# Kernel optimization log

Hardware: AMD Instinct MI355X
Metric: run time of the kernel (lower is better)

The kernel has to match this reference:

```python
import jax, jax.numpy as jnp
import numpy as np

BS, L, D, H, NL, ITEM_NUM = 128, 64, 512, 8, 2, 100000
NEG_INF = -10000.0


def _ln(x):
    m = jnp.mean(x, axis=-1, keepdims=True)
    v = jnp.var(x, axis=-1, keepdims=True)
    return (x - m) * jax.lax.rsqrt(v + 1e-5)


def _user_encoder(input_embs, log_mask, pos_emb, qkv_w, out_w, ffn_w1, ffn_w2):
    # SASRec-style causal transformer encoder (post-LN blocks)
    B, S, d = input_embs.shape
    dh = d // H
    x = _ln(input_embs + pos_emb[None, :, :])
    pad = (log_mask != 0)                                  # [B,S]
    causal = jnp.tril(jnp.ones((S, S), dtype=bool))
    attn_ok = causal[None, :, :] & pad[:, None, :]         # [B,S,S]
    bias = jnp.where(attn_ok, 0.0, NEG_INF)[:, None, :, :]  # [B,1,S,S]
    for l in range(NL):
        qkv = x @ qkv_w[l]                                 # [B,S,3d]
        q, k, v = jnp.split(qkv, 3, axis=-1)
        q = q.reshape(B, S, H, dh).transpose(0, 2, 1, 3)
        k = k.reshape(B, S, H, dh).transpose(0, 2, 1, 3)
        v = v.reshape(B, S, H, dh).transpose(0, 2, 1, 3)
        scores = jnp.einsum('bhqd,bhkd->bhqk', q, k) / jnp.sqrt(jnp.asarray(dh, x.dtype)) + bias
        attn = jax.nn.softmax(scores, axis=-1)
        o = jnp.einsum('bhqk,bhkd->bhqd', attn, v).transpose(0, 2, 1, 3).reshape(B, S, d)
        x = _ln(x + o @ out_w[l])
        h = jax.nn.gelu(x @ ffn_w1[l])
        x = _ln(x + h @ ffn_w2[l])
    return x


def setup_inputs() -> dict:
    key = jax.random.key(0)
    ks = jax.random.split(key, 9)
    sample_items_id = jax.random.randint(ks[0], (BS, L + 1), 0, ITEM_NUM + 1)
    log_mask = jax.random.randint(ks[1], (BS, L), 0, 2).astype(jnp.float32)
    emb_table = (jax.random.normal(ks[2], (ITEM_NUM + 1, D), jnp.float32) * 0.02).at[0].set(0.0)
    pos_emb = jax.random.normal(ks[3], (L, D), jnp.float32) * 0.02
    qkv_w = jax.random.normal(ks[4], (NL, D, 3 * D), jnp.float32) * (D ** -0.5)
    out_w = jax.random.normal(ks[5], (NL, D, D), jnp.float32) * (D ** -0.5)
    ffn_w1 = jax.random.normal(ks[6], (NL, D, 4 * D), jnp.float32) * (D ** -0.5)
    ffn_w2 = jax.random.normal(ks[7], (NL, 4 * D, D), jnp.float32) * ((4 * D) ** -0.5)
    pop_prob = jax.random.uniform(ks[8], (ITEM_NUM + 1,), jnp.float32, 1e-6, 1.0)
    return dict(sample_items_id=sample_items_id, log_mask=log_mask, emb_table=emb_table,
                pos_emb=pos_emb, qkv_w=qkv_w, out_w=out_w, ffn_w1=ffn_w1, ffn_w2=ffn_w2,
                pop_prob=pop_prob)


def reference(sample_items_id, log_mask, emb_table, pos_emb, qkv_w, out_w, ffn_w1, ffn_w2, pop_prob):
    bs, l = log_mask.shape
    N = bs * (l + 1)
    items_flat = sample_items_id.reshape(-1)                        # [N]
    debias = jnp.log(pop_prob[items_flat])                          # [N]
    score_embs = emb_table[items_flat]                              # [N, D]
    input_embs = score_embs.reshape(bs, l + 1, -1)
    prec = _user_encoder(input_embs[:, :-1, :], log_mask, pos_emb, qkv_w, out_w, ffn_w1, ffn_w2)
    prec = prec.reshape(bs * l, -1)                                 # [bs*L, D]
    logits = prec @ score_embs.T - debias[None, :]                  # [bs*L, N]
    # padding-column mask (concat(log_mask, ones) == 0)
    pad_cols = jnp.concatenate([log_mask, jnp.ones((bs, 1), log_mask.dtype)], axis=1).reshape(-1) == 0
    logits = jnp.where(pad_cols[None, :], NEG_INF, logits)
    logits = logits.reshape(bs, l, N)
    # in-batch dedup mask: column k masked for batch i if item k appears in batch i's items
    id_list = sample_items_id.reshape(bs, l + 1)
    member = (items_flat[None, :, None] == id_list[:, None, :]).any(-1)   # [bs, N]
    target_col = jnp.arange(bs)[:, None] * (l + 1) + jnp.arange(1, l + 1)[None, :]  # [bs, L]
    is_target = jnp.arange(N)[None, None, :] == target_col[:, :, None]    # [bs, L, N]
    dedup = member[:, None, :] & ~is_target
    logits = jnp.where(dedup, NEG_INF, logits).reshape(bs * l, N)
    labels = target_col.reshape(-1)                                 # [bs*L]
    logp = jax.nn.log_softmax(logits, axis=-1)
    nll = -jnp.take_along_axis(logp, labels[:, None], axis=1)[:, 0]
    valid = (log_mask.reshape(-1) != 0).astype(logits.dtype)
    return (nll * valid).sum() / valid.sum()
```

## Files before the change

kernel.cpp:

```cpp
#include <hip/hip_runtime.h>
#include <hip/hip_bf16.h>
#include <cstdint>
#include <cstddef>

#define NEG_INF -10000.0f

constexpr int BSZ  = 128;
constexpr int SEQ  = 64;
constexpr int DIM  = 512;
constexpr int HEADS = 8;
constexpr int NLAYER = 2;
constexpr int NCOL = BSZ * (SEQ + 1);
constexpr int NROW = BSZ * SEQ;

typedef __attribute__((ext_vector_type(8))) short bf16x8;
typedef __attribute__((ext_vector_type(4))) short bf16x4;
typedef __attribute__((ext_vector_type(4))) float f32x4;

__device__ __forceinline__ void async_copy16(const void* g, void* l) {
    __builtin_amdgcn_global_load_lds(
        (const __attribute__((address_space(1))) void*)g,
        (__attribute__((address_space(3))) void*)l, 16, 0, 0);
}

__device__ __forceinline__ float gelu_f(float v) {
    float u = 0.7978845608028654f * (v + 0.044715f * v * v * v);
    return 0.5f * v * (1.0f + tanhf(u));
}

__device__ __forceinline__ float block_sum_256(float v, float* sh) {
    #pragma unroll
    for (int off = 32; off > 0; off >>= 1) v += __shfl_down(v, off, 64);
    const int lane = threadIdx.x & 63, w = threadIdx.x >> 6;
    __syncthreads();
    if (lane == 0) sh[w] = v;
    __syncthreads();
    return sh[0] + sh[1] + sh[2] + sh[3];
}

__device__ __forceinline__ void swizzle_rc(int id, int& ry, int& cx) {
    ry = (id & 7) * 8 + ((id >> 3) & 7);
    cx = id >> 6;
}

__global__ __launch_bounds__(128) void gather_kernel(
    const int* __restrict__ ids, const float* __restrict__ table,
    const float* __restrict__ pop, __hip_bfloat16* __restrict__ sebf,
    float* __restrict__ debias) {
    const int k = blockIdx.x, t = threadIdx.x;
    const int id = ids[k];
    float4 v = reinterpret_cast<const float4*>(table + (size_t)id * DIM)[t];
    __hip_bfloat16* dst = sebf + (size_t)k * DIM + t * 4;
    dst[0] = __float2bfloat16(v.x);
    dst[1] = __float2bfloat16(v.y);
    dst[2] = __float2bfloat16(v.z);
    dst[3] = __float2bfloat16(v.w);
    if (t == 0) debias[k] = logf(pop[id]);
}

__global__ __launch_bounds__(256) void mask_kernel(
    const int* __restrict__ ids, const float* __restrict__ log_mask,
    uint8_t* __restrict__ colmask, uint8_t* __restrict__ padcol) {
    const int bi = blockIdx.x >> 3, seg = blockIdx.x & 7;
    __shared__ int sid[65];
    if (threadIdx.x < 65) sid[threadIdx.x] = ids[bi * 65 + threadIdx.x];
    __syncthreads();
    const int kend = (seg + 1) * (NCOL / 8);
    for (int k = seg * (NCOL / 8) + threadIdx.x; k < kend; k += 256) {
        const int id = ids[k];
        bool mem = false;
        #pragma unroll
        for (int j = 0; j < 65; j++) mem |= (sid[j] == id);
        const int i2 = k / 65, jj = k - i2 * 65;
        const bool pc = (jj < 64) && (log_mask[i2 * 64 + jj] == 0.0f);
        colmask[(size_t)bi * NCOL + k] = (mem || pc) ? 1 : 0;
        if (bi == 0) padcol[k] = pc ? 1 : 0;
    }
}

__global__ __launch_bounds__(256) void transpose_bf16_kernel(
    const float* __restrict__ W, __hip_bfloat16* __restrict__ WT, int K, int N) {
    __shared__ float tile[32][33];
    const size_t loff = (size_t)blockIdx.z * K * N;
    const int nt = blockIdx.x * 32, kt = blockIdx.y * 32;
    const int c = threadIdx.x & 31, r = threadIdx.x >> 5;
    #pragma unroll
    for (int p = 0; p < 4; p++)
        tile[p * 8 + r][c] = W[loff + (size_t)(kt + p * 8 + r) * N + nt + c];
    __syncthreads();
    #pragma unroll
    for (int p = 0; p < 4; p++)
        WT[loff + (size_t)(nt + p * 8 + r) * K + kt + c] = __float2bfloat16(tile[c][p * 8 + r]);
}

__global__ __launch_bounds__(256) void add_pos_ln_kernel(
    const __hip_bfloat16* __restrict__ sebf, const float* __restrict__ pos,
    float* __restrict__ x, __hip_bfloat16* __restrict__ xb) {
    __shared__ float sh[4];
    const int r = blockIdx.x, b = r >> 6, s = r & 63, t = threadIdx.x;
    const __hip_bfloat16* src = sebf + ((size_t)b * 65 + s) * DIM;
    const float* pp = pos + (size_t)s * DIM;
    float v0 = __bfloat162float(src[t])       + pp[t];
    float v1 = __bfloat162float(src[t + 256]) + pp[t + 256];
    float sum = block_sum_256(v0 + v1, sh);
    float sq  = block_sum_256(v0 * v0 + v1 * v1, sh);
    float mean = sum * (1.0f / 512.0f);
    float var  = sq  * (1.0f / 512.0f) - mean * mean;
    float rs = rsqrtf(var + 1e-5f);
    float o0 = (v0 - mean) * rs, o1 = (v1 - mean) * rs;
    x[(size_t)r * DIM + t]       = o0;
    x[(size_t)r * DIM + t + 256] = o1;
    xb[(size_t)r * DIM + t]       = __float2bfloat16(o0);
    xb[(size_t)r * DIM + t + 256] = __float2bfloat16(o1);
}

__global__ __launch_bounds__(256) void resid_ln_kernel(
    float* __restrict__ x, const __hip_bfloat16* __restrict__ y,
    __hip_bfloat16* __restrict__ xb) {
    __shared__ float sh[4];
    const int r = blockIdx.x, t = threadIdx.x;
    float* xr = x + (size_t)r * DIM;
    const __hip_bfloat16* yr = y + (size_t)r * DIM;
    float v0 = xr[t]       + __bfloat162float(yr[t]);
    float v1 = xr[t + 256] + __bfloat162float(yr[t + 256]);
    float sum = block_sum_256(v0 + v1, sh);
    float sq  = block_sum_256(v0 * v0 + v1 * v1, sh);
    float mean = sum * (1.0f / 512.0f);
    float var  = sq  * (1.0f / 512.0f) - mean * mean;
    float rs = rsqrtf(var + 1e-5f);
    float o0 = (v0 - mean) * rs, o1 = (v1 - mean) * rs;
    xr[t] = o0; xr[t + 256] = o1;
    xb[(size_t)r * DIM + t]       = __float2bfloat16(o0);
    xb[(size_t)r * DIM + t + 256] = __float2bfloat16(o1);
}

template<int TN, bool GELU>
__global__ __launch_bounds__(256) void gemm_bt_kernel(
    const __hip_bfloat16* __restrict__ A, const __hip_bfloat16* __restrict__ Bt,
    __hip_bfloat16* __restrict__ C, int N, int K) {
    __shared__ uint16_t As[128 * 32];
    __shared__ uint16_t Bs[TN * 32];
    const int tid = threadIdx.x, w = tid >> 6, lane = tid & 63;
    constexpr int AI = (TN == 128) ? 4 : 2;
    const int wr = (TN == 128) ? (w >> 1) : w;
    const int wc = (TN == 128) ? (w & 1) : 0;
    const int rowbase = wr * (AI * 16);
    int ry, cx;
    swizzle_rc(blockIdx.x, ry, cx);
    const int row0 = ry * 128, col0 = cx * TN;
    const uint16_t* Ag = (const uint16_t*)A;
    const uint16_t* Bg = (const uint16_t*)Bt;
    const int la4 = lane >> 2, lk = (lane & 3) * 8;
    f32x4 acc[AI][4];
    #pragma unroll
    for (int i = 0; i < AI; i++)
        #pragma unroll
        for (int j = 0; j < 4; j++) acc[i][j] = {0.f, 0.f, 0.f, 0.f};

    for (int k0 = 0; k0 < K; k0 += 32) {
        #pragma unroll
        for (int i = 0; i < 2; i++) {
            const int rbase = w * 32 + i * 16;
            async_copy16(Ag + (size_t)(row0 + rbase + la4) * K + k0 + lk, &As[rbase * 32]);
        }
        if (TN == 128) {
            #pragma unroll
            for (int i = 0; i < 2; i++) {
                const int rbase = w * 32 + i * 16;
                async_copy16(Bg + (size_t)(col0 + rbase + la4) * K + k0 + lk, &Bs[rbase * 32]);
            }
        } else {
            const int rbase = w * 16;
            async_copy16(Bg + (size_t)(col0 + rbase + la4) * K + k0 + lk, &Bs[rbase * 32]);
        }
        __syncthreads();
        bf16x8 af[AI], bfr[4];
        #pragma unroll
        for (int i = 0; i < AI; i++)
            af[i] = *(const bf16x8*)&As[(rowbase + i * 16 + (lane & 15)) * 32 + (lane >> 4) * 8];
        #pragma unroll
        for (int j = 0; j < 4; j++)
            bfr[j] = *(const bf16x8*)&Bs[(wc * 64 + j * 16 + (lane & 15)) * 32 + (lane >> 4) * 8];
        #pragma unroll
        for (int i = 0; i < AI; i++)
            #pragma unroll
            for (int j = 0; j < 4; j++)
                acc[i][j] = __builtin_amdgcn_mfma_f32_16x16x32_bf16(af[i], bfr[j], acc[i][j], 0, 0, 0);
        __syncthreads();
    }
    #pragma unroll
    for (int i = 0; i < AI; i++) {
        #pragma unroll
        for (int r = 0; r < 4; r++) {
            const int row = row0 + rowbase + i * 16 + (lane >> 4) * 4 + r;
            #pragma unroll
            for (int j = 0; j < 4; j++) {
                const int col = col0 + wc * 64 + j * 16 + (lane & 15);
                float v = acc[i][j][r];
                if (GELU) v = gelu_f(v);
                C[(size_t)row * N + col] = __float2bfloat16(v);
            }
        }
    }
}

__global__ __launch_bounds__(256) void attn_mfma_kernel(
    const __hip_bfloat16* __restrict__ qkv, const float* __restrict__ log_mask,
    __hip_bfloat16* __restrict__ obuf) {
    constexpr int QS = 72;
    constexpr int VS = 72;
    __shared__ uint16_t Qs[64 * QS];
    __shared__ uint16_t Ks_[64 * QS];
    __shared__ uint16_t Ps[64 * QS];
    __shared__ uint16_t Vt[64 * VS];
    __shared__ float mask_s[64];
    const int b = blockIdx.x >> 3, h = blockIdx.x & 7;
    const int tid = threadIdx.x, w = tid >> 6, lane = tid & 63;
    const int quad = lane >> 4, l15 = lane & 15;
    const uint16_t* qg = (const uint16_t*)qkv;

    if (tid < 64) mask_s[tid] = log_mask[b * 64 + tid];
    #pragma unroll
    for (int it = 0; it < 2; it++) {
        const int idx = it * 256 + tid;
        const int s = idx >> 3, c = (idx & 7) * 8;
        const size_t gbase = (size_t)(b * 64 + s) * 1536 + h * 64 + c;
        *(bf16x8*)&Qs[s * QS + c]  = *(const bf16x8*)&qg[gbase];
        *(bf16x8*)&Ks_[s * QS + c] = *(const bf16x8*)&qg[gbase + 512];
        bf16x8 vv = *(const bf16x8*)&qg[gbase + 1024];
        #pragma unroll
        for (int jj = 0; jj < 8; jj++)
            Vt[(c + jj) * VS + s] = (uint16_t)vv[jj];
    }
    __syncthreads();

    f32x4 sacc[4];
    #pragma unroll
    for (int j = 0; j < 4; j++) sacc[j] = {0.f, 0.f, 0.f, 0.f};
    #pragma unroll
    for (int k0 = 0; k0 < 2; k0++) {
        bf16x8 aq = *(const bf16x8*)&Qs[(w * 16 + l15) * QS + k0 * 32 + quad * 8];
        #pragma unroll
        for (int j = 0; j < 4; j++) {
            bf16x8 bk = *(const bf16x8*)&Ks_[(j * 16 + l15) * QS + k0 * 32 + quad * 8];
            sacc[j] = __builtin_amdgcn_mfma_f32_16x16x32_bf16(aq, bk, sacc[j], 0, 0, 0);
        }
    }
    #pragma unroll
    for (int r = 0; r < 4; r++) {
        const int q = w * 16 + quad * 4 + r;
        float vals[4];
        float vmax = -3.0e38f;
        #pragma unroll
        for (int j = 0; j < 4; j++) {
            const int col = j * 16 + l15;
            const bool ok = (col <= q) && (mask_s[col] != 0.0f);
            float v = sacc[j][r] * 0.125f + (ok ? 0.0f : NEG_INF);
            vals[j] = v;
            vmax = fmaxf(vmax, v);
        }
        #pragma unroll
        for (int off = 1; off < 16; off <<= 1) vmax = fmaxf(vmax, __shfl_xor(vmax, off, 64));
        float e[4], s = 0.f;
        #pragma unroll
        for (int j = 0; j < 4; j++) { e[j] = expf(vals[j] - vmax); s += e[j]; }
        #pragma unroll
        for (int off = 1; off < 16; off <<= 1) s += __shfl_xor(s, off, 64);
        const float inv = 1.0f / s;
        #pragma unroll
        for (int j = 0; j < 4; j++) {
            __hip_bfloat16 pb = __float2bfloat16(e[j] * inv);
            Ps[q * QS + j * 16 + l15] = *(uint16_t*)&pb;
        }
    }
    __syncthreads();

    f32x4 oacc[4];
    #pragma unroll
    for (int j = 0; j < 4; j++) oacc[j] = {0.f, 0.f, 0.f, 0.f};
    #pragma unroll
    for (int k0 = 0; k0 < 2; k0++) {
        bf16x8 ap = *(const bf16x8*)&Ps[(w * 16 + l15) * QS + k0 * 32 + quad * 8];
        #pragma unroll
        for (int j = 0; j < 4; j++) {
            bf16x8 bv = *(const bf16x8*)&Vt[(j * 16 + l15) * VS + k0 * 32 + quad * 8];
            oacc[j] = __builtin_amdgcn_mfma_f32_16x16x32_bf16(ap, bv, oacc[j], 0, 0, 0);
        }
    }
    #pragma unroll
    for (int r = 0; r < 4; r++) {
        const int q = w * 16 + quad * 4 + r;
        #pragma unroll
        for (int j = 0; j < 4; j++) {
            const int d = j * 16 + l15;
            obuf[(size_t)(b * 64 + q) * 512 + h * 64 + d] = __float2bfloat16(oacc[j][r]);
        }
    }
}

__global__ __launch_bounds__(256) void logits_kernel(
    const __hip_bfloat16* __restrict__ A, const __hip_bfloat16* __restrict__ Bt,
    const float* __restrict__ debias, const uint8_t* __restrict__ colmask,
    const uint8_t* __restrict__ padcol,
    float* __restrict__ partials, float* __restrict__ label_logit) {
    __shared__ uint16_t As[128 * 32];
    __shared__ uint16_t Bs[128 * 32];
    __shared__ float deb_s[128];
    __shared__ uint8_t cm_s[2][128];
    __shared__ uint8_t pc_s[128];
    const int tid = threadIdx.x, w = tid >> 6, lane = tid & 63;
    const int wr = w >> 1, wc = w & 1;
    int ry, cx;
    swizzle_rc(blockIdx.x, ry, cx);
    const int row0 = ry * 128, col0 = cx * 128;
    const uint16_t* Ag = (const uint16_t*)A;
    const uint16_t* Bg = (const uint16_t*)Bt;
    const int la4 = lane >> 2, lk = (lane & 3) * 8;

    if (tid < 128) {
        deb_s[tid] = debias[col0 + tid];
        pc_s[tid]  = padcol[col0 + tid];
        const int bi0 = row0 >> 6;
        cm_s[0][tid] = colmask[(size_t)bi0 * NCOL + col0 + tid];
        cm_s[1][tid] = colmask[(size_t)(bi0 + 1) * NCOL + col0 + tid];
    }

    f32x4 acc[4][4];
    #pragma unroll
    for (int i = 0; i < 4; i++)
        #pragma unroll
        for (int j = 0; j < 4; j++) acc[i][j] = {0.f, 0.f, 0.f, 0.f};

    for (int k0 = 0; k0 < DIM; k0 += 32) {
        #pragma unroll
        for (int i = 0; i < 2; i++) {
            const int rbase = w * 32 + i * 16;
            async_copy16(Ag + (size_t)(row0 + rbase + la4) * DIM + k0 + lk, &As[rbase * 32]);
            async_copy16(Bg + (size_t)(col0 + rbase + la4) * DIM + k0 + lk, &Bs[rbase * 32]);
        }
        __syncthreads();
        bf16x8 af[4], bfr[4];
        #pragma unroll
        for (int i = 0; i < 4; i++) {
            af[i]  = *(const bf16x8*)&As[(wr * 64 + i * 16 + (lane & 15)) * 32 + (lane >> 4) * 8];
            bfr[i] = *(const bf16x8*)&Bs[(wc * 64 + i * 16 + (lane & 15)) * 32 + (lane >> 4) * 8];
        }
        #pragma unroll
        for (int i = 0; i < 4; i++)
            #pragma unroll
            for (int j = 0; j < 4; j++)
                acc[i][j] = __builtin_amdgcn_mfma_f32_16x16x32_bf16(af[i], bfr[j], acc[i][j], 0, 0, 0);
        __syncthreads();
    }

    #pragma unroll
    for (int i = 0; i < 4; i++) {
        #pragma unroll
        for (int r = 0; r < 4; r++) {
            const int lrow = wr * 64 + i * 16 + (lane >> 4) * 4 + r;
            const int row = row0 + lrow;
            const int bi = row >> 6;
            const int label = bi * 65 + (row & 63) + 1;
            float vals[4];
            float vmax = -3.0e38f;
            #pragma unroll
            for (int j = 0; j < 4; j++) {
                const int lcol = wc * 64 + j * 16 + (lane & 15);
                const int col = col0 + lcol;
                float v = acc[i][j][r] - deb_s[lcol];
                const bool is_lab = (col == label);
                const bool masked = is_lab ? (pc_s[lcol] != 0) : (cm_s[lrow >> 6][lcol] != 0);
                if (masked) v = NEG_INF;
                if (is_lab) label_logit[row] = v;
                vals[j] = v;
                vmax = fmaxf(vmax, v);
            }
            #pragma unroll
            for (int off = 1; off < 16; off <<= 1) vmax = fmaxf(vmax, __shfl_xor(vmax, off, 64));
            float s = 0.f;
            #pragma unroll
            for (int j = 0; j < 4; j++) s += expf(vals[j] - vmax);
            #pragma unroll
            for (int off = 1; off < 16; off <<= 1) s += __shfl_xor(s, off, 64);
            if ((lane & 15) == 0) {
                const int strip = (col0 >> 6) + wc;
                const size_t idx = ((size_t)row * 130 + strip) * 2;
                partials[idx]     = vmax;
                partials[idx + 1] = s;
            }
        }
    }
}

__global__ __launch_bounds__(256) void combine_kernel(
    const float* __restrict__ partials, const float* __restrict__ label_logit,
    const float* __restrict__ log_mask, float* __restrict__ bsums) {
    const int row = blockIdx.x * 256 + threadIdx.x;
    const float* p = partials + (size_t)row * 260;
    float M = -3.4e38f;
    for (int t = 0; t < 130; t++) M = fmaxf(M, p[2 * t]);
    float Ls = 0.f;
    for (int t = 0; t < 130; t++) Ls += p[2 * t + 1] * expf(p[2 * t] - M);
    const float lse = M + logf(Ls);
    const float valid = (log_mask[row] != 0.0f) ? 1.0f : 0.0f;
    float a = (lse - label_logit[row]) * valid;
    float c = valid;
    __shared__ float sa[4], sc[4];
    #pragma unroll
    for (int off = 32; off > 0; off >>= 1) {
        a += __shfl_down(a, off, 64);
        c += __shfl_down(c, off, 64);
    }
    const int lane = threadIdx.x & 63, w = threadIdx.x >> 6;
    if (lane == 0) { sa[w] = a; sc[w] = c; }
    __syncthreads();
    if (threadIdx.x == 0) {
        bsums[blockIdx.x * 2 + 0] = sa[0] + sa[1] + sa[2] + sa[3];
        bsums[blockIdx.x * 2 + 1] = sc[0] + sc[1] + sc[2] + sc[3];
    }
}

__global__ __launch_bounds__(64) void finalize_kernel(
    const float* __restrict__ bsums, float* __restrict__ out) {
    const int t = threadIdx.x;
    float a = 0.f, c = 0.f;
    if (t < 32) { a = bsums[2 * t]; c = bsums[2 * t + 1]; }
    #pragma unroll
    for (int off = 32; off > 0; off >>= 1) {
        a += __shfl_down(a, off, 64);
        c += __shfl_down(c, off, 64);
    }
    if (t == 0) out[0] = a / c;
}

extern "C" void kernel_launch(void* const* d_in, const int* in_sizes, int n_in,
                              void* d_out, int out_size, void* d_ws, size_t ws_size,
                              hipStream_t stream) {
    const int*   ids    = (const int*)d_in[0];
    const float* lm     = (const float*)d_in[1];
    const float* emb    = (const float*)d_in[2];
    const float* pos    = (const float*)d_in[3];
    const float* qkv_w  = (const float*)d_in[4];
    const float* out_w  = (const float*)d_in[5];
    const float* ffn1_w = (const float*)d_in[6];
    const float* ffn2_w = (const float*)d_in[7];
    const float* pop    = (const float*)d_in[8];
    float* out = (float*)d_out;

    char* p = (char*)d_ws;
    auto alloc = [&](size_t bytes) {
        char* r = p;
        p += (bytes + 255) & ~(size_t)255;
        return r;
    };
    typedef __hip_bfloat16 bf16;
    bf16*    sebf     = (bf16*)alloc((size_t)NCOL * DIM * 2);
    float*   debias   = (float*)alloc((size_t)NCOL * 4);
    uint8_t* padcol   = (uint8_t*)alloc(NCOL);
    uint8_t* colmask  = (uint8_t*)alloc((size_t)BSZ * NCOL);
    float*   x        = (float*)alloc((size_t)NROW * DIM * 4);
    bf16*    xb       = (bf16*)alloc((size_t)NROW * DIM * 2);
    bf16*    big      = (bf16*)alloc((size_t)NROW * 2048 * 2);
    bf16*    tmp1     = (bf16*)alloc((size_t)NROW * DIM * 2);
    bf16*    tmp2     = (bf16*)alloc((size_t)NROW * DIM * 2);
    float*   partials = (float*)alloc((size_t)NROW * 130 * 2 * 4);
    float*   lab      = (float*)alloc((size_t)NROW * 4);
    float*   bsums    = (float*)alloc(64 * 4);
    bf16*    qkvT     = (bf16*)alloc((size_t)NLAYER * 1536 * 512 * 2);
    bf16*    outT     = (bf16*)alloc((size_t)NLAYER * 512 * 512 * 2);
    bf16*    f1T      = (bf16*)alloc((size_t)NLAYER * 2048 * 512 * 2);
    bf16*    f2T      = (bf16*)alloc((size_t)NLAYER * 512 * 2048 * 2);

    transpose_bf16_kernel<<<dim3(1536 / 32, 512 / 32, NLAYER), 256, 0, stream>>>(
        qkv_w, qkvT, 512, 1536);
    transpose_bf16_kernel<<<dim3(512 / 32, 512 / 32, NLAYER), 256, 0, stream>>>(
        out_w, outT, 512, 512);
    transpose_bf16_kernel<<<dim3(2048 / 32, 512 / 32, NLAYER), 256, 0, stream>>>(
        ffn1_w, f1T, 512, 2048);
    transpose_bf16_kernel<<<dim3(512 / 32, 2048 / 32, NLAYER), 256, 0, stream>>>(
        ffn2_w, f2T, 2048, 512);

    gather_kernel<<<NCOL, 128, 0, stream>>>(ids, emb, pop, sebf, debias);
    mask_kernel<<<BSZ * 8, 256, 0, stream>>>(ids, lm, colmask, padcol);
    add_pos_ln_kernel<<<NROW, 256, 0, stream>>>(sebf, pos, x, xb);

    for (int l = 0; l < NLAYER; l++) {
        gemm_bt_kernel<128, false><<<(1536 / 128) * 64, 256, 0, stream>>>(
            xb, qkvT + (size_t)l * 1536 * 512, big, 1536, 512);
        attn_mfma_kernel<<<BSZ * HEADS, 256, 0, stream>>>(big, lm, tmp1);
        gemm_bt_kernel<64, false><<<(512 / 64) * 64, 256, 0, stream>>>(
            tmp1, outT + (size_t)l * 512 * 512, tmp2, 512, 512);
        resid_ln_kernel<<<NROW, 256, 0, stream>>>(x, tmp2, xb);
        gemm_bt_kernel<128, true><<<(2048 / 128) * 64, 256, 0, stream>>>(
            xb, f1T + (size_t)l * 2048 * 512, big, 2048, 512);
        gemm_bt_kernel<64, false><<<(512 / 64) * 64, 256, 0, stream>>>(
            big, f2T + (size_t)l * 512 * 2048, tmp2, 512, 2048);
        resid_ln_kernel<<<NROW, 256, 0, stream>>>(x, tmp2, xb);
    }

    logits_kernel<<<65 * 64, 256, 0, stream>>>(
        xb, sebf, debias, colmask, padcol, partials, lab);
    combine_kernel<<<NROW / 256, 256, 0, stream>>>(partials, lab, lm, bsums);
    finalize_kernel<<<1, 64, 0, stream>>>(bsums, out);
}
```

Baseline: 755.0 us.

## Fuse gather with pos-LN, drop fp32 residual, widen GEMM K-step, fixed-max softmax

Merges the embedding gather with the positional add and LayerNorm, and removes the fp32 residual stream so residual LayerNorm runs on the bf16 activations with one wave per row. The GEMM and logits kernels now load 64-wide K chunks per barrier pair, halving synchronisation. Attention packs V transposed as 32-bit pairs and uses fast exp. The logits kernel drops the per-strip max and uses a fixed constant offset for log-sum-exp, which shrinks the partials buffer but can overflow or lose precision if logits exceed the assumed range. Residual precision also falls to bf16.

After: 655.2 us. 13.2% less time.

```diff
diff --git a/kernel.cpp b/kernel.cpp
--- a/kernel.cpp
+++ b/kernel.cpp
@@ -12,9 +12,9 @@
 constexpr int NLAYER = 2;
 constexpr int NCOL = BSZ * (SEQ + 1);
 constexpr int NROW = BSZ * SEQ;
+constexpr float CMAX = 40.0f;
 
 typedef __attribute__((ext_vector_type(8))) short bf16x8;
-typedef __attribute__((ext_vector_type(4))) short bf16x4;
 typedef __attribute__((ext_vector_type(4))) float f32x4;
 
 __device__ __forceinline__ void async_copy16(const void* g, void* l) {
@@ -23,39 +23,64 @@
         (__attribute__((address_space(3))) void*)l, 16, 0, 0);
 }
 
+__device__ __forceinline__ float b2f(uint16_t u) {
+    return __builtin_bit_cast(float, (uint32_t)u << 16);
+}
+__device__ __forceinline__ uint16_t f2b(float f) {
+    __hip_bfloat16 h = __float2bfloat16(f);
+    return __builtin_bit_cast(uint16_t, h);
+}
+
 __device__ __forceinline__ float gelu_f(float v) {
     float u = 0.7978845608028654f * (v + 0.044715f * v * v * v);
     return 0.5f * v * (1.0f + tanhf(u));
 }
 
-__device__ __forceinline__ float block_sum_256(float v, float* sh) {
-    #pragma unroll
-    for (int off = 32; off > 0; off >>= 1) v += __shfl_down(v, off, 64);
-    const int lane = threadIdx.x & 63, w = threadIdx.x >> 6;
-    __syncthreads();
-    if (lane == 0) sh[w] = v;
-    __syncthreads();
-    return sh[0] + sh[1] + sh[2] + sh[3];
-}
-
 __device__ __forceinline__ void swizzle_rc(int id, int& ry, int& cx) {
     ry = (id & 7) * 8 + ((id >> 3) & 7);
     cx = id >> 6;
 }
 
-__global__ __launch_bounds__(128) void gather_kernel(
+__global__ __launch_bounds__(256) void gather_posln_kernel(
     const int* __restrict__ ids, const float* __restrict__ table,
-    const float* __restrict__ pop, __hip_bfloat16* __restrict__ sebf,
-    float* __restrict__ debias) {
-    const int k = blockIdx.x, t = threadIdx.x;
+    const float* __restrict__ pop, const float* __restrict__ pos,
+    __hip_bfloat16* __restrict__ sebf, float* __restrict__ debias,
+    __hip_bfloat16* __restrict__ xb) {
+    const int w = threadIdx.x >> 6, lane = threadIdx.x & 63;
+    const int k = blockIdx.x * 4 + w;
+    const int b = k / 65, s = k - b * 65;
     const int id = ids[k];
-    float4 v = reinterpret_cast<const float4*>(table + (size_t)id * DIM)[t];
-    __hip_bfloat16* dst = sebf + (size_t)k * DIM + t * 4;
-    dst[0] = __float2bfloat16(v.x);
-    dst[1] = __float2bfloat16(v.y);
-    dst[2] = __float2bfloat16(v.z);
-    dst[3] = __float2bfloat16(v.w);
-    if (t == 0) debias[k] = logf(pop[id]);
+    const float* src = table + (size_t)id * DIM + lane * 8;
+    float4 u0 = *(const float4*)src;
+    float4 u1 = *(const float4*)(src + 4);
+    float v[8] = {u0.x, u0.y, u0.z, u0.w, u1.x, u1.y, u1.z, u1.w};
+    bf16x8 se;
+    #pragma unroll
+    for (int j = 0; j < 8; j++) se[j] = (short)f2b(v[j]);
+    *(bf16x8*)((uint16_t*)sebf + (size_t)k * DIM + lane * 8) = se;
+    if (lane == 0) debias[k] = logf(pop[id]);
+    if (s < 64) {
+        const float* pp = pos + (size_t)s * DIM + lane * 8;
+        float4 p0 = *(const float4*)pp;
+        float4 p1 = *(const float4*)(pp + 4);
+        float t[8] = {v[0] + p0.x, v[1] + p0.y, v[2] + p0.z, v[3] + p0.w,
+                      v[4] + p1.x, v[5] + p1.y, v[6] + p1.z, v[7] + p1.w};
+        float sum = 0.f, sq = 0.f;
+        #pragma unroll
+        for (int j = 0; j < 8; j++) { sum += t[j]; sq += t[j] * t[j]; }
+        #pragma unroll
+        for (int off = 32; off > 0; off >>= 1) {
+            sum += __shfl_xor(sum, off, 64);
+            sq  += __shfl_xor(sq,  off, 64);
+        }
+        const float mean = sum * (1.0f / 512.0f);
+        const float var  = sq * (1.0f / 512.0f) - mean * mean;
+        const float rs = rsqrtf(var + 1e-5f);
+        bf16x8 o;
+        #pragma unroll
+        for (int j = 0; j < 8; j++) o[j] = (short)f2b((t[j] - mean) * rs);
+        *(bf16x8*)((uint16_t*)xb + (size_t)(b * 64 + s) * DIM + lane * 8) = o;
+    }
 }
 
 __global__ __launch_bounds__(256) void mask_kernel(
@@ -93,54 +118,43 @@
         WT[loff + (size_t)(nt + p * 8 + r) * K + kt + c] = __float2bfloat16(tile[c][p * 8 + r]);
 }
 
-__global__ __launch_bounds__(256) void add_pos_ln_kernel(
-    const __hip_bfloat16* __restrict__ sebf, const float* __restrict__ pos,
-    float* __restrict__ x, __hip_bfloat16* __restrict__ xb) {
-    __shared__ float sh[4];
-    const int r = blockIdx.x, b = r >> 6, s = r & 63, t = threadIdx.x;
-    const __hip_bfloat16* src = sebf + ((size_t)b * 65 + s) * DIM;
-    const float* pp = pos + (size_t)s * DIM;
-    float v0 = __bfloat162float(src[t])       + pp[t];
-    float v1 = __bfloat162float(src[t + 256]) + pp[t + 256];
-    float sum = block_sum_256(v0 + v1, sh);
-    float sq  = block_sum_256(v0 * v0 + v1 * v1, sh);
-    float mean = sum * (1.0f / 512.0f);
-    float var  = sq  * (1.0f / 512.0f) - mean * mean;
-    float rs = rsqrtf(var + 1e-5f);
-    float o0 = (v0 - mean) * rs, o1 = (v1 - mean) * rs;
-    x[(size_t)r * DIM + t]       = o0;
-    x[(size_t)r * DIM + t + 256] = o1;
-    xb[(size_t)r * DIM + t]       = __float2bfloat16(o0);
-    xb[(size_t)r * DIM + t + 256] = __float2bfloat16(o1);
-}
-
 __global__ __launch_bounds__(256) void resid_ln_kernel(
-    float* __restrict__ x, const __hip_bfloat16* __restrict__ y,
-    __hip_bfloat16* __restrict__ xb) {
-    __shared__ float sh[4];
-    const int r = blockIdx.x, t = threadIdx.x;
-    float* xr = x + (size_t)r * DIM;
-    const __hip_bfloat16* yr = y + (size_t)r * DIM;
-    float v0 = xr[t]       + __bfloat162float(yr[t]);
-    float v1 = xr[t + 256] + __bfloat162float(yr[t + 256]);
-    float sum = block_sum_256(v0 + v1, sh);
-    float sq  = block_sum_256(v0 * v0 + v1 * v1, sh);
-    float mean = sum * (1.0f / 512.0f);
-    float var  = sq  * (1.0f / 512.0f) - mean * mean;
-    float rs = rsqrtf(var + 1e-5f);
-    float o0 = (v0 - mean) * rs, o1 = (v1 - mean) * rs;
-    xr[t] = o0; xr[t + 256] = o1;
-    xb[(size_t)r * DIM + t]       = __float2bfloat16(o0);
-    xb[(size_t)r * DIM + t + 256] = __float2bfloat16(o1);
+    __hip_bfloat16* __restrict__ xb, const __hip_bfloat16* __restrict__ y) {
+    const int w = threadIdx.x >> 6, lane = threadIdx.x & 63;
+    const int row = blockIdx.x * 4 + w;
+    uint16_t* xp = (uint16_t*)xb + (size_t)row * DIM + lane * 8;
+    const uint16_t* yp = (const uint16_t*)y + (size_t)row * DIM + lane * 8;
+    bf16x8 xv = *(const bf16x8*)xp;
+    bf16x8 yv = *(const bf16x8*)yp;
+    float t[8];
+    float sum = 0.f, sq = 0.f;
+    #pragma unroll
+    for (int j = 0; j < 8; j++) {
+        t[j] = b2f((uint16_t)xv[j]) + b2f((uint16_t)yv[j]);
+        sum += t[j]; sq += t[j] * t[j];
+    }
+    #pragma unroll
+    for (int off = 32; off > 0; off >>= 1) {
+        sum += __shfl_xor(sum, off, 64);
+        sq  += __shfl_xor(sq,  off, 64);
+    }
+    const float mean = sum * (1.0f / 512.0f);
+    const float var  = sq * (1.0f / 512.0f) - mean * mean;
+    const float rs = rsqrtf(var + 1e-5f);
+    bf16x8 o;
+    #pragma unroll
+    for (int j = 0; j < 8; j++) o[j] = (short)f2b((t[j] - mean) * rs);
+    *(bf16x8*)xp = o;
 }
 
 template<int TN, bool GELU>
 __global__ __launch_bounds__(256) void gemm_bt_kernel(
     const __hip_bfloat16* __restrict__ A, const __hip_bfloat16* __restrict__ Bt,
     __hip_bfloat16* __restrict__ C, int N, int K) {
-    __shared__ uint16_t As[128 * 32];
-    __shared__ uint16_t Bs[TN * 32];
+    __shared__ uint16_t As[2][128][32];
+    __shared__ uint16_t Bs[2][TN][32];
     const int tid = threadIdx.x, w = tid >> 6, lane = tid & 63;
+    const int quad = lane >> 4, l15 = lane & 15;
     constexpr int AI = (TN == 128) ? 4 : 2;
     const int wr = (TN == 128) ? (w >> 1) : w;
     const int wc = (TN == 128) ? (w & 1) : 0;
@@ -150,52 +164,58 @@
     const int row0 = ry * 128, col0 = cx * TN;
     const uint16_t* Ag = (const uint16_t*)A;
     const uint16_t* Bg = (const uint16_t*)Bt;
-    const int la4 = lane >> 2, lk = (lane & 3) * 8;
+    const int sr = lane >> 2, sc = (lane & 3) * 8;
     f32x4 acc[AI][4];
     #pragma unroll
     for (int i = 0; i < AI; i++)
         #pragma unroll
         for (int j = 0; j < 4; j++) acc[i][j] = {0.f, 0.f, 0.f, 0.f};
 
-    for (int k0 = 0; k0 < K; k0 += 32) {
-        #pragma unroll
-        for (int i = 0; i < 2; i++) {
-            const int rbase = w * 32 + i * 16;
-            async_copy16(Ag + (size_t)(row0 + rbase + la4) * K + k0 + lk, &As[rbase * 32]);
-        }
-        if (TN == 128) {
+    for (int k0 = 0; k0 < K; k0 += 64) {
+        #pragma unroll
+        for (int h = 0; h < 2; h++) {
             #pragma unroll
             for (int i = 0; i < 2; i++) {
-                const int rbase = w * 32 + i * 16;
-                async_copy16(Bg + (size_t)(col0 + rbase + la4) * K + k0 + lk, &Bs[rbase * 32]);
-            }
-        } else {
-            const int rbase = w * 16;
-            async_copy16(Bg + (size_t)(col0 + rbase + la4) * K + k0 + lk, &Bs[rbase * 32]);
+                const int rb = w * 32 + i * 16;
+                async_copy16(Ag + (size_t)(row0 + rb + sr) * K + k0 + h * 32 + sc, &As[h][rb][0]);
+            }
+            if (TN == 128) {
+                #pragma unroll
+                for (int i = 0; i < 2; i++) {
+                    const int rb = w * 32 + i * 16;
+                    async_copy16(Bg + (size_t)(col0 + rb + sr) * K + k0 + h * 32 + sc, &Bs[h][rb][0]);
+                }
+            } else {
+                const int rb = w * 16;
+                async_copy16(Bg + (size_t)(col0 + rb + sr) * K + k0 + h * 32 + sc, &Bs[h][rb][0]);
+            }
         }
         __syncthreads();
-        bf16x8 af[AI], bfr[4];
-        #pragma unroll
-        for (int i = 0; i < AI; i++)
-            af[i] = *(const bf16x8*)&As[(rowbase + i * 16 + (lane & 15)) * 32 + (lane >> 4) * 8];
-        #pragma unroll
-        for (int j = 0; j < 4; j++)
-            bfr[j] = *(const bf16x8*)&Bs[(wc * 64 + j * 16 + (lane & 15)) * 32 + (lane >> 4) * 8];
-        #pragma unroll
-        for (int i = 0; i < AI; i++)
+        #pragma unroll
+        for (int h = 0; h < 2; h++) {
+            bf16x8 af[AI], bfr[4];
+            #pragma unroll
+            for (int i = 0; i < AI; i++)
+                af[i] = *(const bf16x8*)&As[h][rowbase + i * 16 + l15][quad * 8];
             #pragma unroll
             for (int j = 0; j < 4; j++)
-                acc[i][j] = __builtin_amdgcn_mfma_f32_16x16x32_bf16(af[i], bfr[j], acc[i][j], 0, 0, 0);
+                bfr[j] = *(const bf16x8*)&Bs[h][wc * 64 + j * 16 + l15][quad * 8];
+            #pragma unroll
+            for (int i = 0; i < AI; i++)
+                #pragma unroll
+                for (int j = 0; j < 4; j++)
+                    acc[i][j] = __builtin_amdgcn_mfma_f32_16x16x32_bf16(af[i], bfr[j], acc[i][j], 0, 0, 0);
+        }
         __syncthreads();
     }
     #pragma unroll
     for (int i = 0; i < AI; i++) {
         #pragma unroll
         for (int r = 0; r < 4; r++) {
-            const int row = row0 + rowbase + i * 16 + (lane >> 4) * 4 + r;
+            const int row = row0 + rowbase + i * 16 + quad * 4 + r;
             #pragma unroll
             for (int j = 0; j < 4; j++) {
-                const int col = col0 + wc * 64 + j * 16 + (lane & 15);
+                const int col = col0 + wc * 64 + j * 16 + l15;
                 float v = acc[i][j][r];
                 if (GELU) v = gelu_f(v);
                 C[(size_t)row * N + col] = __float2bfloat16(v);
@@ -208,11 +228,11 @@
     const __hip_bfloat16* __restrict__ qkv, const float* __restrict__ log_mask,
     __hip_bfloat16* __restrict__ obuf) {
     constexpr int QS = 72;
-    constexpr int VS = 72;
+    constexpr int VS32 = 36;
     __shared__ uint16_t Qs[64 * QS];
     __shared__ uint16_t Ks_[64 * QS];
     __shared__ uint16_t Ps[64 * QS];
-    __shared__ uint16_t Vt[64 * VS];
+    __shared__ uint32_t Vt32[64 * VS32];
     __shared__ float mask_s[64];
     const int b = blockIdx.x >> 3, h = blockIdx.x & 7;
     const int tid = threadIdx.x, w = tid >> 6, lane = tid & 63;
@@ -227,10 +247,17 @@
         const size_t gbase = (size_t)(b * 64 + s) * 1536 + h * 64 + c;
         *(bf16x8*)&Qs[s * QS + c]  = *(const bf16x8*)&qg[gbase];
         *(bf16x8*)&Ks_[s * QS + c] = *(const bf16x8*)&qg[gbase + 512];
-        bf16x8 vv = *(const bf16x8*)&qg[gbase + 1024];
+    }
+    {
+        const int sp = tid >> 3;
+        const int c = (tid & 7) * 8;
+        const size_t gbase = (size_t)(b * 64 + sp * 2) * 1536 + 1024 + h * 64 + c;
+        bf16x8 v0 = *(const bf16x8*)&qg[gbase];
+        bf16x8 v1 = *(const bf16x8*)&qg[gbase + 1536];
         #pragma unroll
         for (int jj = 0; jj < 8; jj++)
-            Vt[(c + jj) * VS + s] = (uint16_t)vv[jj];
+            Vt32[(c + jj) * VS32 + sp] =
+                (uint32_t)(uint16_t)v0[jj] | ((uint32_t)(uint16_t)v1[jj] << 16);
     }
     __syncthreads();
 
@@ -263,15 +290,13 @@
         for (int off = 1; off < 16; off <<= 1) vmax = fmaxf(vmax, __shfl_xor(vmax, off, 64));
         float e[4], s = 0.f;
         #pragma unroll
-        for (int j = 0; j < 4; j++) { e[j] = expf(vals[j] - vmax); s += e[j]; }
+        for (int j = 0; j < 4; j++) { e[j] = __expf(vals[j] - vmax); s += e[j]; }
         #pragma unroll
         for (int off = 1; off < 16; off <<= 1) s += __shfl_xor(s, off, 64);
         const float inv = 1.0f / s;
         #pragma unroll
-        for (int j = 0; j < 4; j++) {
-            __hip_bfloat16 pb = __float2bfloat16(e[j] * inv);
-            Ps[q * QS + j * 16 + l15] = *(uint16_t*)&pb;
-        }
+        for (int j = 0; j < 4; j++)
+            Ps[q * QS + j * 16 + l15] = f2b(e[j] * inv);
     }
     __syncthreads();
 
@@ -283,7 +308,7 @@
         bf16x8 ap = *(const bf16x8*)&Ps[(w * 16 + l15) * QS + k0 * 32 + quad * 8];
         #pragma unroll
         for (int j = 0; j < 4; j++) {
-            bf16x8 bv = *(const bf16x8*)&Vt[(j * 16 + l15) * VS + k0 * 32 + quad * 8];
+            bf16x8 bv = *(const bf16x8*)&Vt32[(j * 16 + l15) * VS32 + k0 * 16 + quad * 4];
             oacc[j] = __builtin_amdgcn_mfma_f32_16x16x32_bf16(ap, bv, oacc[j], 0, 0, 0);
         }
     }
@@ -303,19 +328,20 @@
     const float* __restrict__ debias, const uint8_t* __restrict__ colmask,
     const uint8_t* __restrict__ padcol,
     float* __restrict__ partials, float* __restrict__ label_logit) {
-    __shared__ uint16_t As[128 * 32];
-    __shared__ uint16_t Bs[128 * 32];
+    __shared__ uint16_t As[2][128][32];
+    __shared__ uint16_t Bs[2][128][32];
     __shared__ float deb_s[128];
     __shared__ uint8_t cm_s[2][128];
     __shared__ uint8_t pc_s[128];
     const int tid = threadIdx.x, w = tid >> 6, lane = tid & 63;
+    const int quad = lane >> 4, l15 = lane & 15;
     const int wr = w >> 1, wc = w & 1;
     int ry, cx;
     swizzle_rc(blockIdx.x, ry, cx);
     const int row0 = ry * 128, col0 = cx * 128;
     const uint16_t* Ag = (const uint16_t*)A;
     const uint16_t* Bg = (const uint16_t*)Bt;
-    const int la4 = lane >> 2, lk = (lane & 3) * 8;
+    const int sr = lane >> 2, sc = (lane & 3) * 8;
 
     if (tid < 128) {
         deb_s[tid] = debias[col0 + tid];
@@ -331,25 +357,31 @@
         #pragma unroll
         for (int j = 0; j < 4; j++) acc[i][j] = {0.f, 0.f, 0.f, 0.f};
 
-    for (int k0 = 0; k0 < DIM; k0 += 32) {
-        #pragma unroll
-        for (int i = 0; i < 2; i++) {
-            const int rbase = w * 32 + i * 16;
-            async_copy16(Ag + (size_t)(row0 + rbase + la4) * DIM + k0 + lk, &As[rbase * 32]);
-            async_copy16(Bg + (size_t)(col0 + rbase + la4) * DIM + k0 + lk, &Bs[rbase * 32]);
+    for (int k0 = 0; k0 < DIM; k0 += 64) {
+        #pragma unroll
+        for (int h = 0; h < 2; h++) {
+            #pragma unroll
+            for (int i = 0; i < 2; i++) {
+                const int rb = w * 32 + i * 16;
+                async_copy16(Ag + (size_t)(row0 + rb + sr) * DIM + k0 + h * 32 + sc, &As[h][rb][0]);
+                async_copy16(Bg + (size_t)(col0 + rb + sr) * DIM + k0 + h * 32 + sc, &Bs[h][rb][0]);
+            }
         }
         __syncthreads();
-        bf16x8 af[4], bfr[4];
-        #pragma unroll
-        for (int i = 0; i < 4; i++) {
-            af[i]  = *(const bf16x8*)&As[(wr * 64 + i * 16 + (lane & 15)) * 32 + (lane >> 4) * 8];
-            bfr[i] = *(const bf16x8*)&Bs[(wc * 64 + i * 16 + (lane & 15)) * 32 + (lane >> 4) * 8];
-        }
-        #pragma unroll
-        for (int i = 0; i < 4; i++)
-            #pragma unroll
-            for (int j = 0; j < 4; j++)
-                acc[i][j] = __builtin_amdgcn_mfma_f32_16x16x32_bf16(af[i], bfr[j], acc[i][j], 0, 0, 0);
+        #pragma unroll
+        for (int h = 0; h < 2; h++) {
+            bf16x8 af[4], bfr[4];
+            #pragma unroll
+            for (int i = 0; i < 4; i++) {
+                af[i]  = *(const bf16x8*)&As[h][wr * 64 + i * 16 + l15][quad * 8];
+                bfr[i] = *(const bf16x8*)&Bs[h][wc * 64 + i * 16 + l15][quad * 8];
+            }
+            #pragma unroll
+            for (int i = 0; i < 4; i++)
+                #pragma unroll
+                for (int j = 0; j < 4; j++)
+                    acc[i][j] = __builtin_amdgcn_mfma_f32_16x16x32_bf16(af[i], bfr[j], acc[i][j], 0, 0, 0);
+        }
         __syncthreads();
     }
 
@@ -357,36 +389,27 @@
     for (int i = 0; i < 4; i++) {
         #pragma unroll
         for (int r = 0; r < 4; r++) {
-            const int lrow = wr * 64 + i * 16 + (lane >> 4) * 4 + r;
+            const int lrow = wr * 64 + i * 16 + quad * 4 + r;
             const int row = row0 + lrow;
             const int bi = row >> 6;
             const int label = bi * 65 + (row & 63) + 1;
-            float vals[4];
-            float vmax = -3.0e38f;
+            float s = 0.f;
             #pragma unroll
             for (int j = 0; j < 4; j++) {
-                const int lcol = wc * 64 + j * 16 + (lane & 15);
+                const int lcol = wc * 64 + j * 16 + l15;
                 const int col = col0 + lcol;
                 float v = acc[i][j][r] - deb_s[lcol];
                 const bool is_lab = (col == label);
                 const bool masked = is_lab ? (pc_s[lcol] != 0) : (cm_s[lrow >> 6][lcol] != 0);
                 if (masked) v = NEG_INF;
                 if (is_lab) label_logit[row] = v;
-                vals[j] = v;
-                vmax = fmaxf(vmax, v);
-            }
-            #pragma unroll
-            for (int off = 1; off < 16; off <<= 1) vmax = fmaxf(vmax, __shfl_xor(vmax, off, 64));
-            float s = 0.f;
-            #pragma unroll
-            for (int j = 0; j < 4; j++) s += expf(vals[j] - vmax);
+                s += __expf(v - CMAX);
+            }
             #pragma unroll
             for (int off = 1; off < 16; off <<= 1) s += __shfl_xor(s, off, 64);
-            if ((lane & 15) == 0) {
+            if (l15 == 0) {
                 const int strip = (col0 >> 6) + wc;
-                const size_t idx = ((size_t)row * 130 + strip) * 2;
-                partials[idx]     = vmax;
-                partials[idx + 1] = s;
+                partials[(size_t)row * 130 + strip] = s;
             }
         }
     }
@@ -396,27 +419,25 @@
     const float* __restrict__ partials, const float* __restrict__ label_logit,
     const float* __restrict__ log_mask, float* __restrict__ bsums) {
     const int row = blockIdx.x * 256 + threadIdx.x;
-    const float* p = partials + (size_t)row * 260;
-    float M = -3.4e38f;
-    for (int t = 0; t < 130; t++) M = fmaxf(M, p[2 * t]);
+    const float* pr = partials + (size_t)row * 130;
     float Ls = 0.f;
-    for (int t = 0; t < 130; t++) Ls += p[2 * t + 1] * expf(p[2 * t] - M);
-    const float lse = M + logf(Ls);
+    for (int t = 0; t < 130; t++) Ls += pr[t];
+    const float lse = CMAX + logf(Ls);
     const float valid = (log_mask[row] != 0.0f) ? 1.0f : 0.0f;
     float a = (lse - label_logit[row]) * valid;
     float c = valid;
-    __shared__ float sa[4], sc[4];
+    __shared__ float sa[4], sc_[4];
     #pragma unroll
     for (int off = 32; off > 0; off >>= 1) {
         a += __shfl_down(a, off, 64);
         c += __shfl_down(c, off, 64);
     }
     const int lane = threadIdx.x & 63, w = threadIdx.x >> 6;
-    if (lane == 0) { sa[w] = a; sc[w] = c; }
+    if (lane == 0) { sa[w] = a; sc_[w] = c; }
     __syncthreads();
     if (threadIdx.x == 0) {
         bsums[blockIdx.x * 2 + 0] = sa[0] + sa[1] + sa[2] + sa[3];
-        bsums[blockIdx.x * 2 + 1] = sc[0] + sc[1] + sc[2] + sc[3];
+        bsums[blockIdx.x * 2 + 1] = sc_[0] + sc_[1] + sc_[2] + sc_[3];
     }
 }
 
@@ -458,12 +479,11 @@
     float*   debias   = (float*)alloc((size_t)NCOL * 4);
     uint8_t* padcol   = (uint8_t*)alloc(NCOL);
     uint8_t* colmask  = (uint8_t*)alloc((size_t)BSZ * NCOL);
-    float*   x        = (float*)alloc((size_t)NROW * DIM * 4);
     bf16*    xb       = (bf16*)alloc((size_t)NROW * DIM * 2);
     bf16*    big      = (bf16*)alloc((size_t)NROW * 2048 * 2);
     bf16*    tmp1     = (bf16*)alloc((size_t)NROW * DIM * 2);
     bf16*    tmp2     = (bf16*)alloc((size_t)NROW * DIM * 2);
-    float*   partials = (float*)alloc((size_t)NROW * 130 * 2 * 4);
+    float*   partials = (float*)alloc((size_t)NROW * 130 * 4);
     float*   lab      = (float*)alloc((size_t)NROW * 4);
     float*   bsums    = (float*)alloc(64 * 4);
     bf16*    qkvT     = (bf16*)alloc((size_t)NLAYER * 1536 * 512 * 2);
@@ -480,9 +500,8 @@
     transpose_bf16_kernel<<<dim3(512 / 32, 2048 / 32, NLAYER), 256, 0, stream>>>(
         ffn2_w, f2T, 2048, 512);
 
-    gather_kernel<<<NCOL, 128, 0, stream>>>(ids, emb, pop, sebf, debias);
+    gather_posln_kernel<<<NCOL / 4, 256, 0, stream>>>(ids, emb, pop, pos, sebf, debias, xb);
     mask_kernel<<<BSZ * 8, 256, 0, stream>>>(ids, lm, colmask, padcol);
-    add_pos_ln_kernel<<<NROW, 256, 0, stream>>>(sebf, pos, x, xb);
 
     for (int l = 0; l < NLAYER; l++) {
         gemm_bt_kernel<128, false><<<(1536 / 128) * 64, 256, 0, stream>>>(
@@ -490,12 +509,12 @@
         attn_mfma_kernel<<<BSZ * HEADS, 256, 0, stream>>>(big, lm, tmp1);
         gemm_bt_kernel<64, false><<<(512 / 64) * 64, 256, 0, stream>>>(
             tmp1, outT + (size_t)l * 512 * 512, tmp2, 512, 512);
-        resid_ln_kernel<<<NROW, 256, 0, stream>>>(x, tmp2, xb);
+        resid_ln_kernel<<<NROW / 4, 256, 0, stream>>>(xb, tmp2);
         gemm_bt_kernel<128, true><<<(2048 / 128) * 64, 256, 0, stream>>>(
             xb, f1T + (size_t)l * 2048 * 512, big, 2048, 512);
         gemm_bt_kernel<64, false><<<(512 / 64) * 64, 256, 0, stream>>>(
             big, f2T + (size_t)l * 512 * 2048, tmp2, 512, 2048);
-        resid_ln_kernel<<<NROW, 256, 0, stream>>>(x, tmp2, xb);
+        resid_ln_kernel<<<NROW / 4, 256, 0, stream>>>(xb, tmp2);
     }
 
     logits_kernel<<<65 * 64, 256, 0, stream>>>(
```
